# Kernel optimization log

Hardware: AMD Instinct MI355X
Metric: run time of the kernel (lower is better)

Reference implementation:

```python
import jax, jax.numpy as jnp
import numpy as np

SQRT_D = 16.0   # sqrt(d), d=256
BETA2 = 18.0    # beta^2 / 2, beta=6
EPS_BN = 1e-5


def _bn1d(x, g, b):
    # eval-mode BatchNorm1d with freshly-initialized running stats (mean=0, var=1)
    scale = g / jnp.sqrt(1.0 + EPS_BN)
    if x.ndim == 3:  # [B, C, N]
        return x * scale[:, None] + b[:, None]
    return x * scale + b  # [B, C]


def _crelu(z):
    return jax.nn.relu(z.real) + 1j * jax.nn.relu(z.imag)


def _sa_layer(x, qk_w, v_w, v_b, t_w, t_b, g, b):
    # x: [B, C, N]; q and k share weights (q_conv.weight = k_conv.weight)
    xq = jnp.einsum('oc,bcn->bno', qk_w, x)            # [B, N, C/4]
    xk = jnp.einsum('oc,bcn->bon', qk_w, x)            # [B, C/4, N]
    xv = jnp.einsum('oc,bcn->bon', v_w, x) + v_b[:, None]
    energy = jnp.einsum('bno,bom->bnm', xq, xk)        # [B, N, N]
    att = jax.nn.softmax(energy, axis=-1)
    att = att / (1e-9 + att.sum(axis=1, keepdims=True))  # sum-normalized over dim=1
    xr = jnp.einsum('bcn,bnm->bcm', xv, att)           # [B, C, N]
    xr = jax.nn.relu(_bn1d(jnp.einsum('oc,bcn->bon', t_w, x - xr) + t_b[:, None], g, b))
    return x + xr


def _forward(x, A, P, cl1_wr, cl1_wi, cl1_br, cl1_bi, cl2_wr, cl2_wi, cl2_br, cl2_bi,
             pt_conv1_w, pt_conv2_w, pt_bn1_g, pt_bn1_b, pt_bn2_g, pt_bn2_b,
             sa_qk_w, sa_v_w, sa_v_b, sa_t_w, sa_t_b, sa_bn_g, sa_bn_b,
             fuse_w, fuse_bn_g, fuse_bn_b, lin1_w, bn6_g, bn6_b,
             lin2_w, lin2_b, bn7_g, bn7_b, lin3_w, lin3_b):
    pts = jnp.transpose(x, (0, 2, 1))                  # [B, N, 3]
    # ---- VecKM: pairwise Gaussian kernel times complex random features ----
    sq = jnp.sum(pts * pts, axis=-1)                   # [B, N]
    D2 = sq[:, :, None] + sq[:, None, :] - 2.0 * jnp.einsum('bnc,bmc->bnm', pts, pts)
    J = jnp.exp(-BETA2 * D2).astype(jnp.complex64)     # [B, N, N]
    eA = jnp.exp(1j * (pts @ A))                       # [B, N, d] complex64
    G = (J @ eA) / eA
    G = G / jnp.linalg.norm(G, axis=-1, keepdims=True) * SQRT_D
    G = G + jnp.exp(1j * (pts @ P))                    # positional encoding
    # ---- ComplexLinear -> ComplexReLU -> ComplexLinear ----
    W1 = (cl1_wr + 1j * cl1_wi).astype(jnp.complex64)
    G = _crelu(G @ W1.T + (cl1_br + 1j * cl1_bi))
    W2 = (cl2_wr + 1j * cl2_wi).astype(jnp.complex64)
    G = G @ W2.T + (cl2_br + 1j * cl2_bi)
    Gr = G.real ** 2 + G.imag ** 2                     # [B, N, 256]
    Gc = jnp.transpose(Gr, (0, 2, 1))                  # [B, 256, N]
    # ---- Point_Transformer_Last ----
    h = jax.nn.relu(_bn1d(jnp.einsum('oc,bcn->bon', pt_conv1_w, Gc), pt_bn1_g, pt_bn1_b))
    h = jax.nn.relu(_bn1d(jnp.einsum('oc,bcn->bon', pt_conv2_w, h), pt_bn2_g, pt_bn2_b))
    feats = []
    for i in range(4):
        h = _sa_layer(h, sa_qk_w[i], sa_v_w[i], sa_v_b[i], sa_t_w[i], sa_t_b[i],
                      sa_bn_g[i], sa_bn_b[i])
        feats.append(h)
    h = jnp.concatenate(feats + [Gc], axis=1)          # [B, 1280, N]
    h = jax.nn.leaky_relu(_bn1d(jnp.einsum('oc,bcn->bon', fuse_w, h), fuse_bn_g, fuse_bn_b), 0.2)
    h = jnp.max(h, axis=-1)                            # adaptive_max_pool1d -> [B, 1024]
    h = jax.nn.leaky_relu(_bn1d(h @ lin1_w.T, bn6_g, bn6_b), 0.2)
    h = jax.nn.leaky_relu(_bn1d(h @ lin2_w.T + lin2_b, bn7_g, bn7_b), 0.2)
    return h @ lin3_w.T + lin3_b                       # [B, 40]


def setup_inputs() -> dict:
    key = jax.random.key(0)
    ks = iter(jax.random.split(key, 64))
    B, N, d = 16, 1024, 256
    r = lambda shape, s=0.05: jax.random.normal(next(ks), shape, dtype=jnp.float32) * s
    inp = {
        'x': jax.random.normal(next(ks), (B, 3, N), dtype=jnp.float32),
        'A': jax.random.normal(next(ks), (3, d), dtype=jnp.float32) * 30.0,
        'P': jax.random.normal(next(ks), (3, d), dtype=jnp.float32),
        'cl1_wr': r((d, d)), 'cl1_wi': r((d, d)), 'cl1_br': r((d,)), 'cl1_bi': r((d,)),
        'cl2_wr': r((d, d)), 'cl2_wi': r((d, d)), 'cl2_br': r((d,)), 'cl2_bi': r((d,)),
        'pt_conv1_w': r((256, 256)), 'pt_conv2_w': r((256, 256)),
        'pt_bn1_g': jnp.ones(256), 'pt_bn1_b': jnp.zeros(256),
        'pt_bn2_g': jnp.ones(256), 'pt_bn2_b': jnp.zeros(256),
        'sa_qk_w': r((4, 64, 256)), 'sa_v_w': r((4, 256, 256)), 'sa_v_b': r((4, 256)),
        'sa_t_w': r((4, 256, 256)), 'sa_t_b': r((4, 256)),
        'sa_bn_g': jnp.ones((4, 256)), 'sa_bn_b': jnp.zeros((4, 256)),
        'fuse_w': r((1024, 1280)), 'fuse_bn_g': jnp.ones(1024), 'fuse_bn_b': jnp.zeros(1024),
        'lin1_w': r((512, 1024)), 'bn6_g': jnp.ones(512), 'bn6_b': jnp.zeros(512),
        'lin2_w': r((256, 512)), 'lin2_b': r((256,)),
        'bn7_g': jnp.ones(256), 'bn7_b': jnp.zeros(256),
        'lin3_w': r((40, 256)), 'lin3_b': r((40,)),
    }
    return inp


def reference(x, A, P, cl1_wr, cl1_wi, cl1_br, cl1_bi, cl2_wr, cl2_wi, cl2_br, cl2_bi,
              pt_conv1_w, pt_conv2_w, pt_bn1_g, pt_bn1_b, pt_bn2_g, pt_bn2_b,
              sa_qk_w, sa_v_w, sa_v_b, sa_t_w, sa_t_b, sa_bn_g, sa_bn_b,
              fuse_w, fuse_bn_g, fuse_bn_b, lin1_w, bn6_g, bn6_b,
              lin2_w, lin2_b, bn7_g, bn7_b, lin3_w, lin3_b):
    return _forward(x, A, P, cl1_wr, cl1_wi, cl1_br, cl1_bi, cl2_wr, cl2_wi, cl2_br, cl2_bi,
                    pt_conv1_w, pt_conv2_w, pt_bn1_g, pt_bn1_b, pt_bn2_g, pt_bn2_b,
                    sa_qk_w, sa_v_w, sa_v_b, sa_t_w, sa_t_b, sa_bn_g, sa_bn_b,
                    fuse_w, fuse_bn_g, fuse_bn_b, lin1_w, bn6_g, bn6_b,
                    lin2_w, lin2_b, bn7_g, bn7_b, lin3_w, lin3_b)
```

## Files before the change

### kernel.cpp

```cpp
#include <hip/hip_runtime.h>
#include <math.h>

#define BB 16
#define NN 1024
#define DD 256

typedef unsigned short u16;
typedef unsigned int uint32;
typedef __attribute__((ext_vector_type(8))) short s8v;
typedef __attribute__((ext_vector_type(4))) float f4v;

__device__ __forceinline__ u16 f2b(float f) {
  uint32 u = __float_as_uint(f);
  return (u16)((u + 0x7fffu + ((u >> 16) & 1u)) >> 16);
}
__device__ __forceinline__ float b2f(u16 u) {
  return __uint_as_float(((uint32)u) << 16);
}
__device__ __forceinline__ float blo(uint32 w) { return __uint_as_float(w << 16); }
__device__ __forceinline__ float bhi(uint32 w) { return __uint_as_float(w & 0xffff0000u); }

__device__ __forceinline__ float waveRedSum(float v) {
  #pragma unroll
  for (int o = 32; o; o >>= 1) v += __shfl_xor(v, o, 64);
  return v;
}
__device__ __forceinline__ float waveRedMax(float v) {
  #pragma unroll
  for (int o = 32; o; o >>= 1) v = fmaxf(v, __shfl_xor(v, o, 64));
  return v;
}

__global__ void k_pts(const float* __restrict__ x, float* __restrict__ pts) {
  int i = blockIdx.x * 256 + threadIdx.x;
  if (i >= BB * NN) return;
  int b = i >> 10, n = i & 1023;
  const float* xb = x + (size_t)b * 3 * NN;
  pts[i * 3 + 0] = xb[n];
  pts[i * 3 + 1] = xb[NN + n];
  pts[i * 3 + 2] = xb[2 * NN + n];
}

__global__ void k_phase(const float* __restrict__ pts, const float* __restrict__ A,
                        float2* __restrict__ eA) {
  int i = blockIdx.x * 256 + threadIdx.x;
  int d = i & 255; int bn = i >> 8;
  float p0 = pts[bn * 3], p1 = pts[bn * 3 + 1], p2 = pts[bn * 3 + 2];
  float ta = p0 * A[d] + p1 * A[256 + d] + p2 * A[512 + d];
  float s, c;
  sincosf(ta, &s, &c); eA[i] = make_float2(c, s);
}

__global__ void k_eat(const float2* __restrict__ eA, u16* __restrict__ eAT) {
  int bid = blockIdx.x;
  int dt = bid & 7, nt = (bid >> 3) & 15, b = bid >> 7;
  int d0 = dt * 32, n0 = nt * 64;
  __shared__ u16 cosT[32][72], sinT[32][72];
  int t = threadIdx.x;
  {
    int n = t >> 2, dg = (t & 3) * 8;
    const float2* p = eA + ((size_t)(b * 1024 + n0 + n)) * 256 + d0 + dg;
    #pragma unroll
    for (int j = 0; j < 8; j++) {
      float2 v = p[j];
      cosT[dg + j][n] = f2b(v.x);
      sinT[dg + j][n] = f2b(v.y);
    }
  }
  __syncthreads();
  {
    int rr = t >> 2, ng = (t & 3) * 16;
    int d = rr >> 1, cmp = rr & 1;
    const u16* src = (cmp ? &sinT[d][ng] : &cosT[d][ng]);
    uint4 v0 = *(const uint4*)src;
    uint4 v1 = *(const uint4*)(src + 8);
    u16* dst = eAT + ((size_t)(b * 512 + 2 * d0 + rr)) * 1024 + n0 + ng;
    *(uint4*)dst = v0;
    *(uint4*)(dst + 8) = v1;
  }
}

__global__ void k_jbuild(const float* __restrict__ pts, u16* __restrict__ J) {
  int bid = blockIdx.x;
  int b = bid >> 10, n = bid & 1023;
  int t = threadIdx.x;
  const float* pb = pts + (size_t)b * 3072;
  float pnx = pb[n * 3], pny = pb[n * 3 + 1], pnz = pb[n * 3 + 2];
  int m = t * 4;
  const float* pm = pb + (size_t)m * 3;
  float4 a = *(const float4*)pm;
  float4 bq = *(const float4*)(pm + 4);
  float4 c = *(const float4*)(pm + 8);
  float dx, dy, dz, d2;
  dx = a.x - pnx;  dy = a.y - pny;  dz = a.z - pnz;  d2 = dx*dx + dy*dy + dz*dz;
  float j0 = __expf(-18.0f * d2);
  dx = a.w - pnx;  dy = bq.x - pny; dz = bq.y - pnz; d2 = dx*dx + dy*dy + dz*dz;
  float j1 = __expf(-18.0f * d2);
  dx = bq.z - pnx; dy = bq.w - pny; dz = c.x - pnz;  d2 = dx*dx + dy*dy + dz*dz;
  float j2 = __expf(-18.0f * d2);
  dx = c.y - pnx;  dy = c.z - pny;  dz = c.w - pnz;  d2 = dx*dx + dy*dy + dz*dz;
  float j3 = __expf(-18.0f * d2);
  uint32 lo = (uint32)f2b(j0) | ((uint32)f2b(j1) << 16);
  uint32 hi = (uint32)f2b(j2) | ((uint32)f2b(j3) << 16);
  *(uint2*)(J + (size_t)bid * 1024 + m) = make_uint2(lo, hi);
}

__global__ void k_norm(const float2* __restrict__ M, const float2* __restrict__ eA,
                       const float* __restrict__ pts, const float* __restrict__ P,
                       u16* __restrict__ Gb) {
  int bn = blockIdx.x; int c = threadIdx.x;
  size_t idx = (size_t)bn * DD + c;
  float2 m = M[idx], e = eA[idx];
  float gr = m.x * e.x + m.y * e.y;
  float gi = m.y * e.x - m.x * e.y;
  float s = gr * gr + gi * gi;
  s = waveRedSum(s);
  __shared__ float red[4];
  if ((c & 63) == 0) red[c >> 6] = s;
  __syncthreads();
  float tot = red[0] + red[1] + red[2] + red[3];
  float scale = 16.0f / sqrtf(tot);
  float p0 = pts[bn * 3], p1 = pts[bn * 3 + 1], p2 = pts[bn * 3 + 2];
  float tp = p0 * P[c] + p1 * P[256 + c] + p2 * P[512 + c];
  float sp, cp; sincosf(tp, &sp, &cp);
  uint32 pk = (uint32)f2b(gr * scale + cp) | ((uint32)f2b(gi * scale + sp) << 16);
  *(uint32*)(Gb + idx * 2) = pk;
}

__global__ void k_cast(const float* __restrict__ s, u16* __restrict__ d, int n) {
  int i = blockIdx.x * 256 + threadIdx.x;
  if (i < n) d[i] = f2b(s[i]);
}
__global__ void k_wprep(const float* __restrict__ wr, const float* __restrict__ wi,
                        u16* __restrict__ dst) {
  int i = blockIdx.x * 256 + threadIdx.x;
  int op = i >> 9, c2 = i & 511, c = c2 >> 1, pl = c2 & 1;
  float v;
  if (op < 256) v = pl ? -wi[op * 256 + c] : wr[op * 256 + c];
  else          v = pl ?  wr[(op - 256) * 256 + c] : wi[(op - 256) * 256 + c];
  dst[i] = f2b(v);
}
__global__ void k_cbias(const float* __restrict__ br, const float* __restrict__ bi,
                        float* __restrict__ cb) {
  int t = threadIdx.x;
  cb[t] = (t < 256) ? br[t] : bi[t - 256];
}

__global__ void k_g2(const u16* __restrict__ G2b, u16* __restrict__ bigT) {
  int i = blockIdx.x * 256 + threadIdx.x;
  int row = i >> 8, c = i & 255;
  float re = b2f(G2b[(size_t)row * 512 + 2 * c]);
  float im = b2f(G2b[(size_t)row * 512 + 2 * c + 1]);
  bigT[(size_t)row * 1280 + 1024 + c] = f2b(re * re + im * im);
}

template<int BM>
__launch_bounds__(256)
__global__ void k_mm(const u16* __restrict__ Ab, long a_bs, int lda,
                     const u16* __restrict__ Btb, long b_bs, int ldb,
                     int K, int tiles_m, int tiles_n,
                     const float* __restrict__ bias,
                     const float* __restrict__ bng, const float* __restrict__ bnb,
                     const float* __restrict__ cbias,
                     int act,
                     const float* __restrict__ res, long res_bs, int res_sub,
                     float* __restrict__ outF, long outF_bs, int ldF,
                     u16* __restrict__ outB, long outB_bs, int ldBo, int ileave,
                     u16* __restrict__ outT, long outT_bs, int ldT,
                     float* __restrict__ outPool) {
  constexpr int BN = 128;
  constexpr int WM = (BM == 128) ? 64 : 32;
  constexpr int MI = WM / 16;
  __shared__ u16 smem[BN * BM];
  u16* As = smem;
  u16* Bs = smem + BM * 32;
  int t = threadIdx.x;
  int l = t & 63, w = t >> 6;
  int p = l & 15, q = l >> 4;
  int bid = blockIdx.x;
  int tn = bid % tiles_n;
  int tm = (bid / tiles_n) % tiles_m;
  int b  = bid / (tiles_n * tiles_m);
  int m0 = tm * BM, n0 = tn * BN;
  int wm = w >> 1, wn = w & 1;
  const u16* Ap = Ab + (size_t)b * a_bs;
  const u16* Bp = Btb + (size_t)b * b_bs;

  f4v acc[MI][4];
  #pragma unroll
  for (int i = 0; i < MI; i++)
    #pragma unroll
    for (int j = 0; j < 4; j++) acc[i][j] = (f4v){0.f, 0.f, 0.f, 0.f};

  int arow = t >> 2, kg = (t & 3) * 8;
  for (int k0 = 0; k0 < K; k0 += 32) {
    __syncthreads();
    #pragma unroll
    for (int it = 0; it < BM / 64; it++) {
      int r = it * 64 + arow;
      float4 v = *(const float4*)(Ap + (size_t)(m0 + r) * lda + k0 + kg);
      *(float4*)&As[r * 32 + kg] = v;
    }
    #pragma unroll
    for (int it = 0; it < 2; it++) {
      int r = it * 64 + arow;
      float4 v = *(const float4*)(Bp + (size_t)(n0 + r) * ldb + k0 + kg);
      *(float4*)&Bs[r * 32 + kg] = v;
    }
    __syncthreads();
    s8v af[MI], bf[4];
    #pragma unroll
    for (int i = 0; i < MI; i++)
      af[i] = *(const s8v*)&As[(wm * WM + i * 16 + p) * 32 + q * 8];
    #pragma unroll
    for (int j = 0; j < 4; j++)
      bf[j] = *(const s8v*)&Bs[(wn * 64 + j * 16 + p) * 32 + q * 8];
    #pragma unroll
    for (int i = 0; i < MI; i++)
      #pragma unroll
      for (int j = 0; j < 4; j++)
        acc[i][j] = __builtin_amdgcn_mfma_f32_16x16x32_bf16(af[i], bf[j], acc[i][j], 0, 0, 0);
  }

  __syncthreads();

  float cbv[4];
  #pragma unroll
  for (int j = 0; j < 4; j++) {
    int no = n0 + wn * 64 + j * 16 + p;
    cbv[j] = cbias ? cbias[no] : 0.0f;
  }
  float pmax[MI][4];
  #pragma unroll
  for (int i = 0; i < MI; i++)
    #pragma unroll
    for (int r = 0; r < 4; r++) pmax[i][r] = -3.0e38f;
  const float BNS = 0.99999500003749966f;
  #pragma unroll
  for (int i = 0; i < MI; i++) {
    #pragma unroll
    for (int r = 0; r < 4; r++) {
      int mo = m0 + wm * WM + i * 16 + q * 4 + r;
      float mult = 1.f, add = 0.f;
      if (bias) add = bias[mo];
      if (bng) { float s = bng[mo] * BNS; add = add * s + bnb[mo]; mult = s; }
      #pragma unroll
      for (int j = 0; j < 4; j++) {
        int no = n0 + wn * 64 + j * 16 + p;
        float v = acc[i][j][r];
        v = v * mult + add;
        if (cbias) v += cbv[j];
        if (act == 1) v = fmaxf(v, 0.f);
        else if (act == 2) v = v > 0.f ? v : 0.2f * v;
        if (res) {
          float rv = res[(size_t)b * res_bs + (size_t)mo * NN + no];
          v = res_sub ? rv - v : rv + v;
        }
        if (outPool) pmax[i][r] = fmaxf(pmax[i][r], v);
        if (outF) outF[(size_t)b * outF_bs + (size_t)mo * ldF + no] = v;
        if (outB) {
          int noo = ileave ? (((no & 255) << 1) | (no >> 8)) : no;
          outB[(size_t)b * outB_bs + (size_t)mo * ldBo + noo] = f2b(v);
        }
        if (outT) smem[(wn * 64 + j * 16 + p) * BM + (mo - m0)] = f2b(v);
      }
    }
  }
  if (outT) {
    __syncthreads();
    constexpr int CPR = BM / 8;
    constexpr int RPP = 256 / CPR;
    int row0 = t / CPR, cg = (t % CPR) * 8;
    for (int rr = row0; rr < BN; rr += RPP) {
      float4 v = *(const float4*)&smem[rr * BM + cg];
      *(float4*)(outT + (size_t)b * outT_bs + (size_t)(n0 + rr) * ldT + m0 + cg) = v;
    }
  }
  if (outPool) {
    float* pf = (float*)smem;
    #pragma unroll
    for (int i = 0; i < MI; i++)
      #pragma unroll
      for (int r = 0; r < 4; r++) {
        float m = pmax[i][r];
        #pragma unroll
        for (int o = 1; o < 16; o <<= 1) m = fmaxf(m, __shfl_xor(m, o, 64));
        if (p == 0) pf[(wm * WM + i * 16 + q * 4 + r) * 2 + wn] = m;
      }
    __syncthreads();
    if (t < BM) {
      float mv = fmaxf(pf[t * 2], pf[t * 2 + 1]);
      outPool[((size_t)b * (tiles_m * BM) + m0 + t) * tiles_n + tn] = mv;
    }
  }
}

__global__ void k_rowstats(const u16* __restrict__ E, float* __restrict__ rmax_,
                           float* __restrict__ rinv_) {
  int row = blockIdx.x;
  const u16* pp = E + (size_t)row * NN;
  int t = threadIdx.x;
  uint2 wv = *(const uint2*)(pp + t * 4);
  float v0 = blo(wv.x), v1 = bhi(wv.x), v2 = blo(wv.y), v3 = bhi(wv.y);
  float mx = fmaxf(fmaxf(v0, v1), fmaxf(v2, v3));
  mx = waveRedMax(mx);
  __shared__ float redm[4];
  __shared__ float reds[4];
  if ((t & 63) == 0) redm[t >> 6] = mx;
  __syncthreads();
  mx = fmaxf(fmaxf(redm[0], redm[1]), fmaxf(redm[2], redm[3]));
  float s = __expf(v0 - mx) + __expf(v1 - mx) + __expf(v2 - mx) + __expf(v3 - mx);
  s = waveRedSum(s);
  if ((t & 63) == 0) reds[t >> 6] = s;
  __syncthreads();
  if (t == 0) {
    float tot = reds[0] + reds[1] + reds[2] + reds[3];
    rmax_[row] = mx;
    rinv_[row] = 1.0f / tot;
  }
}

__launch_bounds__(256)
__global__ void k_xratt(const u16* __restrict__ xv_, const u16* __restrict__ E,
                        const float* __restrict__ rmax_, const float* __restrict__ rinv_,
                        const float* __restrict__ XinF, long xinF_bs,
                        u16* __restrict__ diffT) {
  __shared__ u16 smem[16384];
  __shared__ float colred[128][4];
  u16* As = smem;
  u16* Bs = smem + 4096;
  int t = threadIdx.x;
  int l = t & 63, w = t >> 6;
  int p = l & 15, q = l >> 4;
  int bid = blockIdx.x;
  int mt = bid & 7, ct = (bid >> 3) & 1, b = bid >> 4;
  int c0 = ct * 128, m0 = mt * 128;
  int wm = w >> 1, wn = w & 1;
  const u16* Ap = xv_ + (size_t)b * 262144;
  const u16* Ep = E + ((size_t)b << 20);
  const float* rmx = rmax_ + (b << 10);
  const float* riv = rinv_ + (b << 10);
  f4v acc[4][4];
  #pragma unroll
  for (int i = 0; i < 4; i++)
    #pragma unroll
    for (int j = 0; j < 4; j++) acc[i][j] = (f4v){0.f, 0.f, 0.f, 0.f};
  float colpart0 = 0.f, colpart1 = 0.f;
  int arow = t >> 2, kg = (t & 3) * 8;
  for (int k0 = 0; k0 < 1024; k0 += 32) {
    __syncthreads();
    #pragma unroll
    for (int it = 0; it < 2; it++) {
      int r = it * 64 + arow;
      *(float4*)&As[r * 32 + kg] = *(const float4*)(Ap + (size_t)(c0 + r) * 1024 + k0 + kg);
    }
    float4 ma0 = *(const float4*)(rmx + k0 + kg);
    float4 ma1 = *(const float4*)(rmx + k0 + kg + 4);
    float4 ia0 = *(const float4*)(riv + k0 + kg);
    float4 ia1 = *(const float4*)(riv + k0 + kg + 4);
    #pragma unroll
    for (int it = 0; it < 2; it++) {
      int r = it * 64 + arow;
      uint4 e8 = *(const uint4*)(Ep + (size_t)(m0 + r) * 1024 + k0 + kg);
      float p0 = __expf(blo(e8.x) - ma0.x) * ia0.x;
      float p1 = __expf(bhi(e8.x) - ma0.y) * ia0.y;
      float p2 = __expf(blo(e8.y) - ma0.z) * ia0.z;
      float p3 = __expf(bhi(e8.y) - ma0.w) * ia0.w;
      float p4 = __expf(blo(e8.z) - ma1.x) * ia1.x;
      float p5 = __expf(bhi(e8.z) - ma1.y) * ia1.y;
      float p6 = __expf(blo(e8.w) - ma1.z) * ia1.z;
      float p7 = __expf(bhi(e8.w) - ma1.w) * ia1.w;
      float s8 = ((p0 + p1) + (p2 + p3)) + ((p4 + p5) + (p6 + p7));
      if (it == 0) colpart0 += s8; else colpart1 += s8;
      uint32 w0 = (uint32)f2b(p0) | ((uint32)f2b(p1) << 16);
      uint32 w1 = (uint32)f2b(p2) | ((uint32)f2b(p3) << 16);
      uint32 w2 = (uint32)f2b(p4) | ((uint32)f2b(p5) << 16);
      uint32 w3 = (uint32)f2b(p6) | ((uint32)f2b(p7) << 16);
      *(uint4*)&Bs[r * 32 + kg] = make_uint4(w0, w1, w2, w3);
    }
    __syncthreads();
    s8v af[4], bf[4];
    #pragma unroll
    for (int i = 0; i < 4; i++)
      af[i] = *(const s8v*)&As[(wm * 64 + i * 16 + p) * 32 + q * 8];
    #pragma unroll
    for (int j = 0; j < 4; j++)
      bf[j] = *(const s8v*)&Bs[(wn * 64 + j * 16 + p) * 32 + q * 8];
    #pragma unroll
    for (int i = 0; i < 4; i++)
      #pragma unroll
      for (int j = 0; j < 4; j++)
        acc[i][j] = __builtin_amdgcn_mfma_f32_16x16x32_bf16(af[i], bf[j], acc[i][j], 0, 0, 0);
  }
  colred[arow][t & 3] = colpart0;
  colred[64 + arow][t & 3] = colpart1;
  __syncthreads();
  float csv[4];
  #pragma unroll
  for (int j = 0; j < 4; j++) {
    int ml = wn * 64 + j * 16 + p;
    csv[j] = 1.0f / (1e-9f + colred[ml][0] + colred[ml][1] + colred[ml][2] + colred[ml][3]);
  }
  #pragma unroll
  for (int i = 0; i < 4; i++) {
    #pragma unroll
    for (int r = 0; r < 4; r++) {
      int cl = wm * 64 + i * 16 + q * 4 + r;
      int c = c0 + cl;
      #pragma unroll
      for (int j = 0; j < 4; j++) {
        int ml = wn * 64 + j * 16 + p;
        float v = acc[i][j][r] * csv[j];
        float rv = XinF[(size_t)b * xinF_bs + (size_t)c * 1024 + m0 + ml];
        smem[ml * 128 + cl] = f2b(rv - v);
      }
    }
  }
  __syncthreads();
  int rr0 = t >> 4, cg = (t & 15) * 8;
  #pragma unroll
  for (int k = 0; k < 8; k++) {
    int rr = rr0 + k * 16;
    *(float4*)(diffT + (size_t)b * 262144 + (size_t)(m0 + rr) * 256 + c0 + cg) =
        *(const float4*)&smem[rr * 128 + cg];
  }
}

__global__ void k_pool8(const float* __restrict__ pp, float* __restrict__ pool) {
  int i = blockIdx.x * 256 + threadIdx.x;
  const float4* p4 = (const float4*)(pp + (size_t)i * 8);
  float4 a = p4[0], b = p4[1];
  pool[i] = fmaxf(fmaxf(fmaxf(a.x, a.y), fmaxf(a.z, a.w)),
                  fmaxf(fmaxf(b.x, b.y), fmaxf(b.z, b.w)));
}

__global__ void k_fc(const float* __restrict__ in, int Cc,
                     const float* __restrict__ W,
                     const float* __restrict__ bias,
                     const float* __restrict__ bng, const float* __restrict__ bnb,
                     int act, float* __restrict__ out, int O) {
  int i = blockIdx.x * 256 + threadIdx.x;
  if (i >= BB * O) return;
  int b = i / O, o = i % O;
  const float* xp = in + (size_t)b * Cc;
  const float* wp = W + (size_t)o * Cc;
  float s = 0.f;
  for (int c = 0; c < Cc; c += 4) {
    float4 xv = *(const float4*)(xp + c);
    float4 wv = *(const float4*)(wp + c);
    s += xv.x * wv.x + xv.y * wv.y + xv.z * wv.z + xv.w * wv.w;
  }
  if (bias) s += bias[o];
  const float BNS = 0.99999500003749966f;
  if (bng) s = s * (bng[o] * BNS) + bnb[o];
  if (act == 2) s = s > 0.f ? s : 0.2f * s;
  else if (act == 1) s = fmaxf(s, 0.f);
  out[i] = s;
}

extern "C" void kernel_launch(void* const* d_in, const int* in_sizes, int n_in,
                              void* d_out, int out_size, void* d_ws, size_t ws_size,
                              hipStream_t stream) {
  const float* x        = (const float*)d_in[0];
  const float* A        = (const float*)d_in[1];
  const float* P        = (const float*)d_in[2];
  const float* cl1_wr   = (const float*)d_in[3];
  const float* cl1_wi   = (const float*)d_in[4];
  const float* cl1_br   = (const float*)d_in[5];
  const float* cl1_bi   = (const float*)d_in[6];
  const float* cl2_wr   = (const float*)d_in[7];
  const float* cl2_wi   = (const float*)d_in[8];
  const float* cl2_br   = (const float*)d_in[9];
  const float* cl2_bi   = (const float*)d_in[10];
  const float* pt_c1_w  = (const float*)d_in[11];
  const float* pt_c2_w  = (const float*)d_in[12];
  const float* pt_bn1_g = (const float*)d_in[13];
  const float* pt_bn1_b = (const float*)d_in[14];
  const float* pt_bn2_g = (const float*)d_in[15];
  const float* pt_bn2_b = (const float*)d_in[16];
  const float* sa_qk_w  = (const float*)d_in[17];
  const float* sa_v_w   = (const float*)d_in[18];
  const float* sa_v_b   = (const float*)d_in[19];
  const float* sa_t_w   = (const float*)d_in[20];
  const float* sa_t_b   = (const float*)d_in[21];
  const float* sa_bn_g  = (const float*)d_in[22];
  const float* sa_bn_b  = (const float*)d_in[23];
  const float* fuse_w   = (const float*)d_in[24];
  const float* fuse_g   = (const float*)d_in[25];
  const float* fuse_b   = (const float*)d_in[26];
  const float* lin1_w   = (const float*)d_in[27];
  const float* bn6_g    = (const float*)d_in[28];
  const float* bn6_b    = (const float*)d_in[29];
  const float* lin2_w   = (const float*)d_in[30];
  const float* lin2_b   = (const float*)d_in[31];
  const float* bn7_g    = (const float*)d_in[32];
  const float* bn7_b    = (const float*)d_in[33];
  const float* lin3_w   = (const float*)d_in[34];
  const float* lin3_b   = (const float*)d_in[35];

  float* ws = (float*)d_ws;
  const size_t oPts  = 0;
  const size_t oS    = 65536;
  const size_t oBigT = oS + 16777216;
  const size_t oXf0  = oBigT + 10485760;
  const size_t oXf1  = oXf0 + 4194304;
  const size_t oH1T  = oXf1 + 4194304;
  const size_t oH2T  = oH1T + 2097152;
  const size_t oXkT  = oH2T + 2097152;
  const size_t oXv   = oXkT + 524288;
  const size_t oAux  = oXv + 2097152;
  const size_t oGb   = oAux + 8388608;
  const size_t oW1c  = oGb + 4194304;
  const size_t oW2c  = oW1c + 131072;
  const size_t oCb1  = oW2c + 131072;
  const size_t oCb2  = oCb1 + 512;
  const size_t oPool = oCb2 + 512;
  const size_t oFc1  = oPool + 16384;
  const size_t oFc2  = oFc1 + 8192;
  const size_t oWp   = oFc2 + 4096;

  float*  pts  = ws + oPts;
  float2* eA   = (float2*)(ws + oS);
  float2* Mj   = (float2*)(ws + oS + 8388608);
  u16*    G1b  = (u16*)(ws + oS);
  u16*    G2b  = (u16*)(ws + oS + 8388608);
  u16*    Eb   = (u16*)(ws + oS);
  float*  poolP= ws + oS + 8388608;
  u16*    bigT = (u16*)(ws + oBigT);
  float*  Xf0  = ws + oXf0;
  float*  Xf1  = ws + oXf1;
  u16*    h1T  = (u16*)(ws + oH1T);
  u16*    diffT= (u16*)(ws + oH1T);
  u16*    h2T  = (u16*)(ws + oH2T);
  u16*    xkT  = (u16*)(ws + oXkT);
  u16*    xv   = (u16*)(ws + oXv);
  u16*    eAT  = (u16*)(ws + oAux);
  u16*    Jb   = (u16*)(ws + oAux + 4194304);
  float*  rmax = ws + oAux;
  float*  rinv = ws + oAux + 16384;
  u16*    Gb   = (u16*)(ws + oGb);
  u16*    W1c  = (u16*)(ws + oW1c);
  u16*    W2c  = (u16*)(ws + oW2c);
  float*  cb1  = ws + oCb1;
  float*  cb2  = ws + oCb2;
  float*  pool = ws + oPool;
  float*  fc1  = ws + oFc1;
  float*  fc2  = ws + oFc2;
  u16*    wp   = (u16*)(ws + oWp);
  u16* wp_pt1  = wp;
  u16* wp_pt2  = wp + 65536;
  u16* wp_qk   = wp + 131072;
  u16* wp_v    = wp + 196608;
  u16* wp_t    = wp + 458752;
  u16* wp_fuse = wp + 720896;

  k_cast<<<256, 256, 0, stream>>>(pt_c1_w, wp_pt1, 65536);
  k_cast<<<256, 256, 0, stream>>>(pt_c2_w, wp_pt2, 65536);
  k_cast<<<256, 256, 0, stream>>>(sa_qk_w, wp_qk, 65536);
  k_cast<<<1024, 256, 0, stream>>>(sa_v_w, wp_v, 262144);
  k_cast<<<1024, 256, 0, stream>>>(sa_t_w, wp_t, 262144);
  k_cast<<<5120, 256, 0, stream>>>(fuse_w, wp_fuse, 1310720);
  k_wprep<<<1024, 256, 0, stream>>>(cl1_wr, cl1_wi, W1c);
  k_wprep<<<1024, 256, 0, stream>>>(cl2_wr, cl2_wi, W2c);
  k_cbias<<<1, 512, 0, stream>>>(cl1_br, cl1_bi, cb1);
  k_cbias<<<1, 512, 0, stream>>>(cl2_br, cl2_bi, cb2);

  k_pts<<<64, 256, 0, stream>>>(x, pts);
  k_phase<<<16384, 256, 0, stream>>>(pts, A, eA);
  k_eat<<<2048, 256, 0, stream>>>(eA, eAT);
  k_jbuild<<<16384, 256, 0, stream>>>(pts, Jb);
  k_mm<128><<<512, 256, 0, stream>>>(Jb, 1048576, 1024, eAT, 524288, 1024, 1024, 8, 4,
      nullptr, nullptr, nullptr, nullptr, 0, nullptr, 0, 0,
      (float*)Mj, 524288, 512, nullptr, 0, 0, 0, nullptr, 0, 0, nullptr);
  k_norm<<<BB * NN, 256, 0, stream>>>(Mj, eA, pts, P, Gb);

  k_mm<128><<<512, 256, 0, stream>>>(Gb, 0, 512, W1c, 0, 512, 512, 128, 4,
      nullptr, nullptr, nullptr, cb1, 1, nullptr, 0, 0,
      nullptr, 0, 0, G1b, 0, 512, 1, nullptr, 0, 0, nullptr);
  k_mm<128><<<512, 256, 0, stream>>>(G1b, 0, 512, W2c, 0, 512, 512, 128, 4,
      nullptr, nullptr, nullptr, cb2, 0, nullptr, 0, 0,
      nullptr, 0, 0, G2b, 0, 512, 1, nullptr, 0, 0, nullptr);
  k_g2<<<16384, 256, 0, stream>>>(G2b, bigT);

  const long bsBigT = 1310720;
  const long bsH256 = 262144;
  const long bsXkT  = 65536;
  const long bsXvU  = 262144;
  const long bsF    = 262144;
  const long bsEU   = 1048576;

  k_mm<128><<<256, 256, 0, stream>>>(wp_pt1, 0, 256, bigT + 1024, bsBigT, 1280, 256, 2, 8,
      nullptr, pt_bn1_g, pt_bn1_b, nullptr, 1, nullptr, 0, 0,
      nullptr, 0, 0, nullptr, 0, 0, 0, h1T, bsH256, 256, nullptr);
  k_mm<128><<<256, 256, 0, stream>>>(wp_pt2, 0, 256, h1T, bsH256, 256, 256, 2, 8,
      nullptr, pt_bn2_g, pt_bn2_b, nullptr, 1, nullptr, 0, 0,
      Xf0, bsF, 1024, nullptr, 0, 0, 0, h2T, bsH256, 256, nullptr);

  for (int i = 0; i < 4; i++) {
    const u16* XinT   = (i == 0) ? h2T : (bigT + (i - 1) * 256);
    long       xinT_bs= (i == 0) ? bsH256 : bsBigT;
    int        xinT_ld= (i == 0) ? 256 : 1280;
    float*     XinF   = (i & 1) ? Xf1 : Xf0;
    float*     XoutF  = (i & 1) ? Xf0 : Xf1;
    const u16* qkw = wp_qk + (size_t)i * 16384;
    const u16* vw  = wp_v + (size_t)i * 65536;
    const u16* tw  = wp_t + (size_t)i * 65536;

    k_mm<64><<<128, 256, 0, stream>>>(qkw, 0, 256, XinT, xinT_bs, xinT_ld, 256, 1, 8,
        nullptr, nullptr, nullptr, nullptr, 0, nullptr, 0, 0,
        nullptr, 0, 0, nullptr, 0, 0, 0, xkT, bsXkT, 64, nullptr);
    k_mm<128><<<256, 256, 0, stream>>>(vw, 0, 256, XinT, xinT_bs, xinT_ld, 256, 2, 8,
        sa_v_b + i * 256, nullptr, nullptr, nullptr, 0, nullptr, 0, 0,
        nullptr, 0, 0, xv, bsXvU, 1024, 0, nullptr, 0, 0, nullptr);
    k_mm<128><<<1024, 256, 0, stream>>>(xkT, bsXkT, 64, xkT, bsXkT, 64, 64, 8, 8,
        nullptr, nullptr, nullptr, nullptr, 0, nullptr, 0, 0,
        nullptr, 0, 0, Eb, bsEU, 1024, 0, nullptr, 0, 0, nullptr);
    k_rowstats<<<BB * NN, 256, 0, stream>>>(Eb, rmax, rinv);
    k_xratt<<<256, 256, 0, stream>>>(xv, Eb, rmax, rinv, XinF, bsF, diffT);
    k_mm<128><<<256, 256, 0, stream>>>(tw, 0, 256, diffT, bsH256, 256, 256, 2, 8,
        sa_t_b + i * 256, sa_bn_g + i * 256, sa_bn_b + i * 256, nullptr, 1,
        XinF, bsF, 0,
        XoutF, bsF, 1024, nullptr, 0, 0, 0, bigT + i * 256, bsBigT, 1280, nullptr);
  }

  k_mm<128><<<1024, 256, 0, stream>>>(wp_fuse, 0, 1280, bigT, bsBigT, 1280, 1280, 8, 8,
      nullptr, fuse_g, fuse_b, nullptr, 2, nullptr, 0, 0,
      nullptr, 0, 0, nullptr, 0, 0, 0, nullptr, 0, 0, poolP);
  k_pool8<<<64, 256, 0, stream>>>(poolP, pool);

  k_fc<<<32, 256, 0, stream>>>(pool, 1024, lin1_w, nullptr, bn6_g, bn6_b, 2, fc1, 512);
  k_fc<<<16, 256, 0, stream>>>(fc1, 512, lin2_w, lin2_b, bn7_g, bn7_b, 2, fc2, 256);
  k_fc<<<3, 256, 0, stream>>>(fc2, 256, lin3_w, lin3_b, nullptr, nullptr, 0, (float*)d_out, 40);
}
```

Measured before the change: 1.105 ms.

## Fuse softmax row statistics into energy GEMM epilogue and drop rowstats kernel

```diff
diff --git a/kernel.cpp b/kernel.cpp
--- a/kernel.cpp
+++ b/kernel.cpp
@@ -167,7 +167,8 @@
                      float* __restrict__ outF, long outF_bs, int ldF,
                      u16* __restrict__ outB, long outB_bs, int ldBo, int ileave,
                      u16* __restrict__ outT, long outT_bs, int ldT,
-                     float* __restrict__ outPool) {
+                     float* __restrict__ outPool,
+                     float* __restrict__ outStats) {
   constexpr int BN = 128;
   constexpr int WM = (BM == 128) ? 64 : 32;
   constexpr int MI = WM / 16;
@@ -290,43 +291,53 @@
     __syncthreads();
     if (t < BM) {
       float mv = fmaxf(pf[t * 2], pf[t * 2 + 1]);
-      outPool[((size_t)b * (tiles_m * BM) + m0 + t) * tiles_n + tn] = mv;
-    }
-  }
-}
-
-__global__ void k_rowstats(const u16* __restrict__ E, float* __restrict__ rmax_,
-                           float* __restrict__ rinv_) {
-  int row = blockIdx.x;
-  const u16* pp = E + (size_t)row * NN;
-  int t = threadIdx.x;
-  uint2 wv = *(const uint2*)(pp + t * 4);
-  float v0 = blo(wv.x), v1 = bhi(wv.x), v2 = blo(wv.y), v3 = bhi(wv.y);
-  float mx = fmaxf(fmaxf(v0, v1), fmaxf(v2, v3));
-  mx = waveRedMax(mx);
-  __shared__ float redm[4];
-  __shared__ float reds[4];
-  if ((t & 63) == 0) redm[t >> 6] = mx;
-  __syncthreads();
-  mx = fmaxf(fmaxf(redm[0], redm[1]), fmaxf(redm[2], redm[3]));
-  float s = __expf(v0 - mx) + __expf(v1 - mx) + __expf(v2 - mx) + __expf(v3 - mx);
-  s = waveRedSum(s);
-  if ((t & 63) == 0) reds[t >> 6] = s;
-  __syncthreads();
-  if (t == 0) {
-    float tot = reds[0] + reds[1] + reds[2] + reds[3];
-    rmax_[row] = mx;
-    rinv_[row] = 1.0f / tot;
+      outPool[((size_t)b * tiles_n + tn) * (size_t)(tiles_m * BM) + m0 + t] = mv;
+    }
+  }
+  if (outStats) {
+    float* sm1 = (float*)smem;
+    float* sm2 = sm1 + BM * 2;
+    #pragma unroll
+    for (int i = 0; i < MI; i++)
+      #pragma unroll
+      for (int r = 0; r < 4; r++) {
+        float m = fmaxf(fmaxf(acc[i][0][r], acc[i][1][r]), fmaxf(acc[i][2][r], acc[i][3][r]));
+        #pragma unroll
+        for (int o = 1; o < 16; o <<= 1) m = fmaxf(m, __shfl_xor(m, o, 64));
+        if (p == 0) sm1[(wm * WM + i * 16 + q * 4 + r) * 2 + wn] = m;
+      }
+    __syncthreads();
+    #pragma unroll
+    for (int i = 0; i < MI; i++)
+      #pragma unroll
+      for (int r = 0; r < 4; r++) {
+        int row = wm * WM + i * 16 + q * 4 + r;
+        float g = fmaxf(sm1[row * 2], sm1[row * 2 + 1]);
+        float s = __expf(acc[i][0][r] - g) + __expf(acc[i][1][r] - g) +
+                  __expf(acc[i][2][r] - g) + __expf(acc[i][3][r] - g);
+        #pragma unroll
+        for (int o = 1; o < 16; o <<= 1) s += __shfl_xor(s, o, 64);
+        if (p == 0) sm2[row * 2 + wn] = s;
+      }
+    __syncthreads();
+    if (t < BM) {
+      float g = fmaxf(sm1[t * 2], sm1[t * 2 + 1]);
+      float ssum = sm2[t * 2] + sm2[t * 2 + 1];
+      *(float2*)(outStats + (((size_t)b * (tiles_m * BM) + m0 + t) * tiles_n + tn) * 2)
+          = make_float2(g, ssum);
+    }
   }
 }
 
 __launch_bounds__(256)
 __global__ void k_xratt(const u16* __restrict__ xv_, const u16* __restrict__ E,
-                        const float* __restrict__ rmax_, const float* __restrict__ rinv_,
+                        const float* __restrict__ part_,
                         const float* __restrict__ XinF, long xinF_bs,
                         u16* __restrict__ diffT) {
   __shared__ u16 smem[16384];
   __shared__ float colred[128][4];
+  __shared__ float rmS[1024];
+  __shared__ float riS[1024];
   u16* As = smem;
   u16* Bs = smem + 4096;
   int t = threadIdx.x;
@@ -338,8 +349,23 @@
   int wm = w >> 1, wn = w & 1;
   const u16* Ap = xv_ + (size_t)b * 262144;
   const u16* Ep = E + ((size_t)b << 20);
-  const float* rmx = rmax_ + (b << 10);
-  const float* riv = rinv_ + (b << 10);
+  {
+    const float2* pbase = (const float2*)(part_ + (size_t)b * 16384);
+    for (int row = t; row < 1024; row += 256) {
+      const float2* pp = pbase + row * 8;
+      float2 vv[8];
+      #pragma unroll
+      for (int k = 0; k < 8; k++) vv[k] = pp[k];
+      float g = vv[0].x;
+      #pragma unroll
+      for (int k = 1; k < 8; k++) g = fmaxf(g, vv[k].x);
+      float s = 0.f;
+      #pragma unroll
+      for (int k = 0; k < 8; k++) s += vv[k].y * __expf(vv[k].x - g);
+      rmS[row] = g;
+      riS[row] = 1.0f / s;
+    }
+  }
   f4v acc[4][4];
   #pragma unroll
   for (int i = 0; i < 4; i++)
@@ -354,10 +380,10 @@
       int r = it * 64 + arow;
       *(float4*)&As[r * 32 + kg] = *(const float4*)(Ap + (size_t)(c0 + r) * 1024 + k0 + kg);
     }
-    float4 ma0 = *(const float4*)(rmx + k0 + kg);
-    float4 ma1 = *(const float4*)(rmx + k0 + kg + 4);
-    float4 ia0 = *(const float4*)(riv + k0 + kg);
-    float4 ia1 = *(const float4*)(riv + k0 + kg + 4);
+    float4 ma0 = *(const float4*)&rmS[k0 + kg];
+    float4 ma1 = *(const float4*)&rmS[k0 + kg + 4];
+    float4 ia0 = *(const float4*)&riS[k0 + kg];
+    float4 ia1 = *(const float4*)&riS[k0 + kg + 4];
     #pragma unroll
     for (int it = 0; it < 2; it++) {
       int r = it * 64 + arow;
@@ -428,10 +454,12 @@
 
 __global__ void k_pool8(const float* __restrict__ pp, float* __restrict__ pool) {
   int i = blockIdx.x * 256 + threadIdx.x;
-  const float4* p4 = (const float4*)(pp + (size_t)i * 8);
-  float4 a = p4[0], b = p4[1];
-  pool[i] = fmaxf(fmaxf(fmaxf(a.x, a.y), fmaxf(a.z, a.w)),
-                  fmaxf(fmaxf(b.x, b.y), fmaxf(b.z, b.w)));
+  int b = i >> 10, o = i & 1023;
+  const float* base = pp + (size_t)b * 8192 + o;
+  float m = base[0];
+  #pragma unroll
+  for (int tn = 1; tn < 8; tn++) m = fmaxf(m, base[tn * 1024]);
+  pool[i] = m;
 }
 
 __global__ void k_fc(const float* __restrict__ in, int Cc,
@@ -536,8 +564,7 @@
   u16*    xv   = (u16*)(ws + oXv);
   u16*    eAT  = (u16*)(ws + oAux);
   u16*    Jb   = (u16*)(ws + oAux + 4194304);
-  float*  rmax = ws + oAux;
-  float*  rinv = ws + oAux + 16384;
+  float*  partP= ws + oAux;
   u16*    Gb   = (u16*)(ws + oGb);
   u16*    W1c  = (u16*)(ws + oW1c);
   u16*    W2c  = (u16*)(ws + oW2c);
@@ -571,15 +598,15 @@
   k_jbuild<<<16384, 256, 0, stream>>>(pts, Jb);
   k_mm<128><<<512, 256, 0, stream>>>(Jb, 1048576, 1024, eAT, 524288, 1024, 1024, 8, 4,
       nullptr, nullptr, nullptr, nullptr, 0, nullptr, 0, 0,
-      (float*)Mj, 524288, 512, nullptr, 0, 0, 0, nullptr, 0, 0, nullptr);
+      (float*)Mj, 524288, 512, nullptr, 0, 0, 0, nullptr, 0, 0, nullptr, nullptr);
   k_norm<<<BB * NN, 256, 0, stream>>>(Mj, eA, pts, P, Gb);
 
   k_mm<128><<<512, 256, 0, stream>>>(Gb, 0, 512, W1c, 0, 512, 512, 128, 4,
       nullptr, nullptr, nullptr, cb1, 1, nullptr, 0, 0,
-      nullptr, 0, 0, G1b, 0, 512, 1, nullptr, 0, 0, nullptr);
+      nullptr, 0, 0, G1b, 0, 512, 1, nullptr, 0, 0, nullptr, nullptr);
   k_mm<128><<<512, 256, 0, stream>>>(G1b, 0, 512, W2c, 0, 512, 512, 128, 4,
       nullptr, nullptr, nullptr, cb2, 0, nullptr, 0, 0,
-      nullptr, 0, 0, G2b, 0, 512, 1, nullptr, 0, 0, nullptr);
+      nullptr, 0, 0, G2b, 0, 512, 1, nullptr, 0, 0, nullptr, nullptr);
   k_g2<<<16384, 256, 0, stream>>>(G2b, bigT);
 
   const long bsBigT = 1310720;
@@ -591,10 +618,10 @@
 
   k_mm<128><<<256, 256, 0, stream>>>(wp_pt1, 0, 256, bigT + 1024, bsBigT, 1280, 256, 2, 8,
       nullptr, pt_bn1_g, pt_bn1_b, nullptr, 1, nullptr, 0, 0,
-      nullptr, 0, 0, nullptr, 0, 0, 0, h1T, bsH256, 256, nullptr);
+      nullptr, 0, 0, nullptr, 0, 0, 0, h1T, bsH256, 256, nullptr, nullptr);
   k_mm<128><<<256, 256, 0, stream>>>(wp_pt2, 0, 256, h1T, bsH256, 256, 256, 2, 8,
       nullptr, pt_bn2_g, pt_bn2_b, nullptr, 1, nullptr, 0, 0,
-      Xf0, bsF, 1024, nullptr, 0, 0, 0, h2T, bsH256, 256, nullptr);
+      Xf0, bsF, 1024, nullptr, 0, 0, 0, h2T, bsH256, 256, nullptr, nullptr);
 
   for (int i = 0; i < 4; i++) {
     const u16* XinT   = (i == 0) ? h2T : (bigT + (i - 1) * 256);
@@ -608,24 +635,23 @@
 
     k_mm<64><<<128, 256, 0, stream>>>(qkw, 0, 256, XinT, xinT_bs, xinT_ld, 256, 1, 8,
         nullptr, nullptr, nullptr, nullptr, 0, nullptr, 0, 0,
-        nullptr, 0, 0, nullptr, 0, 0, 0, xkT, bsXkT, 64, nullptr);
+        nullptr, 0, 0, nullptr, 0, 0, 0, xkT, bsXkT, 64, nullptr, nullptr);
     k_mm<128><<<256, 256, 0, stream>>>(vw, 0, 256, XinT, xinT_bs, xinT_ld, 256, 2, 8,
         sa_v_b + i * 256, nullptr, nullptr, nullptr, 0, nullptr, 0, 0,
-        nullptr, 0, 0, xv, bsXvU, 1024, 0, nullptr, 0, 0, nullptr);
+        nullptr, 0, 0, xv, bsXvU, 1024, 0, nullptr, 0, 0, nullptr, nullptr);
     k_mm<128><<<1024, 256, 0, stream>>>(xkT, bsXkT, 64, xkT, bsXkT, 64, 64, 8, 8,
         nullptr, nullptr, nullptr, nullptr, 0, nullptr, 0, 0,
-        nullptr, 0, 0, Eb, bsEU, 1024, 0, nullptr, 0, 0, nullptr);
-    k_rowstats<<<BB * NN, 256, 0, stream>>>(Eb, rmax, rinv);
-    k_xratt<<<256, 256, 0, stream>>>(xv, Eb, rmax, rinv, XinF, bsF, diffT);
+        nullptr, 0, 0, Eb, bsEU, 1024, 0, nullptr, 0, 0, nullptr, partP);
+    k_xratt<<<256, 256, 0, stream>>>(xv, Eb, partP, XinF, bsF, diffT);
     k_mm<128><<<256, 256, 0, stream>>>(tw, 0, 256, diffT, bsH256, 256, 256, 2, 8,
         sa_t_b + i * 256, sa_bn_g + i * 256, sa_bn_b + i * 256, nullptr, 1,
         XinF, bsF, 0,
-        XoutF, bsF, 1024, nullptr, 0, 0, 0, bigT + i * 256, bsBigT, 1280, nullptr);
+        XoutF, bsF, 1024, nullptr, 0, 0, 0, bigT + i * 256, bsBigT, 1280, nullptr, nullptr);
   }
 
   k_mm<128><<<1024, 256, 0, stream>>>(wp_fuse, 0, 1280, bigT, bsBigT, 1280, 1280, 8, 8,
       nullptr, fuse_g, fuse_b, nullptr, 2, nullptr, 0, 0,
-      nullptr, 0, 0, nullptr, 0, 0, 0, nullptr, 0, 0, poolP);
+      nullptr, 0, 0, nullptr, 0, 0, 0, nullptr, 0, 0, poolP, nullptr);
   k_pool8<<<64, 256, 0, stream>>>(poolP, pool);
 
   k_fc<<<32, 256, 0, stream>>>(pool, 1024, lin1_w, nullptr, bn6_g, bn6_b, 2, fc1, 512);
```

New measurement: 1.079 ms. 2.4% less time.
